# Kernel tuning notes

Measured on AMD Instinct MI355X. Metric: run time of the kernel, lower is better.

## Reference

```python
import jax, jax.numpy as jnp
import numpy as np

N_NODES = 50000
N_GRAPHS = 1024


def _linear_params(key, fan_in, fan_out):
    k1, k2 = jax.random.split(key)
    lim = 1.0 / np.sqrt(fan_in)
    W = jax.random.uniform(k1, (fan_in, fan_out), minval=-lim, maxval=lim, dtype=jnp.float32)
    b = jax.random.uniform(k2, (fan_out,), minval=-lim, maxval=lim, dtype=jnp.float32)
    return W, b


def gcn_conv(x, W, b, src, dst, n):
    # PyG GCNConv: D^{-1/2} (A + I) D^{-1/2} X W + b, deg counted at target after self-loops
    h = x @ W                                   # [N, out]
    deg = jnp.zeros((n,), h.dtype).at[dst].add(1.0) + 1.0
    dinv = jax.lax.rsqrt(deg)
    norm = dinv[src] * dinv[dst]                # [E]
    msg = h[src] * norm[:, None]                # [E, out] (dominant traffic)
    agg = jax.ops.segment_sum(msg, dst, num_segments=n)
    agg = agg + h * (dinv * dinv)[:, None]      # self-loop contribution
    return agg + b


def setup_inputs() -> dict:
    key = jax.random.key(0)
    ks = jax.random.split(key, 16)
    x = jax.random.normal(ks[0], (N_NODES, 64), dtype=jnp.float32)
    edge_index = jax.random.randint(ks[1], (2, 800000), 0, N_NODES, dtype=jnp.int64)
    batch = jnp.sort(jax.random.randint(ks[2], (N_NODES,), 0, N_GRAPHS, dtype=jnp.int64))
    fingerprint_features = jax.random.uniform(ks[3], (N_GRAPHS, 2048), dtype=jnp.float32)
    func_groups = jax.random.uniform(ks[4], (N_GRAPHS, 167), dtype=jnp.float32)
    W1, b1 = _linear_params(ks[5], 64, 128)
    W2, b2 = _linear_params(ks[6], 128, 256)
    W3, b3 = _linear_params(ks[7], 256, 256)
    Wr1, br1 = _linear_params(ks[8], 128, 256)
    Wr2, br2 = _linear_params(ks[9], 256, 256)
    Wfp, bfp = _linear_params(ks[10], 2048, 256)
    Wfg, bfg = _linear_params(ks[11], 167, 256)
    attn_W = jax.random.uniform(ks[12], (256, 256), dtype=jnp.float32)
    Wfc, bfc = _linear_params(ks[13], 256, 1)
    return dict(x=x, edge_index=edge_index, batch=batch,
                fingerprint_features=fingerprint_features, func_groups=func_groups,
                W1=W1, b1=b1, W2=W2, b2=b2, W3=W3, b3=b3,
                Wr1=Wr1, br1=br1, Wr2=Wr2, br2=br2,
                Wfp=Wfp, bfp=bfp, Wfg=Wfg, bfg=bfg,
                attn_W=attn_W, Wfc=Wfc, bfc=bfc)


def reference(x, edge_index, batch, fingerprint_features, func_groups,
              W1, b1, W2, b2, W3, b3, Wr1, br1, Wr2, br2,
              Wfp, bfp, Wfg, bfg, attn_W, Wfc, bfc):
    n = x.shape[0]
    src, dst = edge_index[0], edge_index[1]
    x1 = jax.nn.relu(gcn_conv(x, W1, b1, src, dst, n))            # [N,128]
    # dropout inactive (eval mode)
    x2 = jax.nn.relu(gcn_conv(x1, W2, b2, src, dst, n) + x1 @ Wr1 + br1)  # [N,256]
    x3 = jax.nn.relu(gcn_conv(x2, W3, b3, src, dst, n) + x2 @ Wr2 + br2)  # [N,256]
    fp = jax.nn.relu(fingerprint_features @ Wfp + bfp)            # [B,256]
    fg = jax.nn.relu(func_groups @ Wfg + bfg)                     # [B,256]
    attn = jax.nn.softmax(x3 @ attn_W, axis=1)                    # [N,256]
    xw = attn * x3
    sums = jax.ops.segment_sum(xw, batch, num_segments=N_GRAPHS)  # [B,256]
    cnt = jax.ops.segment_sum(jnp.ones((n,), xw.dtype), batch, num_segments=N_GRAPHS)
    pooled = sums / jnp.maximum(cnt, 1.0)[:, None]                # global_mean_pool
    out = (pooled + fp + fg) @ Wfc + bfc                          # [B,1]
    return out.reshape(-1, 1)
```

## Files before the change

### kernel.cpp

```cpp
#include <hip/hip_runtime.h>
#include <math.h>

#define CDIV(a,b) (((a)+(b)-1)/(b))

typedef __attribute__((ext_vector_type(8))) short bf16x8;
typedef __attribute__((ext_vector_type(4))) float f32x4;

__device__ inline unsigned short f2bf(float f) {
    unsigned int u = __float_as_uint(f);
    u += 0x7fffu + ((u >> 16) & 1u);
    return (unsigned short)(u >> 16);
}
__device__ inline float bf2f(unsigned short h) { return __uint_as_float(((unsigned int)h) << 16); }

__global__ void deg_count_kernel(const int* __restrict__ dst, int* __restrict__ deg, int E) {
    int e = blockIdx.x * blockDim.x + threadIdx.x;
    if (e < E) atomicAdd(&deg[dst[e]], 1);
}

__global__ void dinv_kernel(const int* __restrict__ deg, float* __restrict__ dinv, int N) {
    int i = blockIdx.x * blockDim.x + threadIdx.x;
    if (i < N) dinv[i] = rsqrtf((float)deg[i] + 1.0f);
}

__global__ void scan_kernel(const int* __restrict__ deg, int* __restrict__ off, int N, int E) {
    __shared__ int wsum[16];
    __shared__ int carry_s;
    const int t = threadIdx.x;
    const int lane = t & 63, wid = t >> 6;
    if (t == 0) carry_s = 0;
    __syncthreads();
    for (int base = 0; base < N; base += 1024) {
        int i = base + t;
        int v = (i < N) ? deg[i] : 0;
        int x = v;
        #pragma unroll
        for (int ofs = 1; ofs < 64; ofs <<= 1) {
            int y = __shfl_up(x, ofs, 64);
            if (lane >= ofs) x += y;
        }
        if (lane == 63) wsum[wid] = x;
        __syncthreads();
        if (wid == 0) {
            int wv = (lane < 16) ? wsum[lane] : 0;
            #pragma unroll
            for (int ofs = 1; ofs < 16; ofs <<= 1) {
                int y = __shfl_up(wv, ofs, 64);
                if (lane >= ofs) wv += y;
            }
            if (lane < 16) wsum[lane] = wv;
        }
        __syncthreads();
        int carry = carry_s;
        int wexcl = (wid == 0) ? 0 : wsum[wid - 1];
        int incl = x + wexcl;
        if (i < N) off[i] = carry + incl - v;
        __syncthreads();
        if (t == 1023) carry_s = carry + incl;
        __syncthreads();
    }
    if (t == 0) off[N] = E;
}

__global__ void csr_fill_kernel(const int* __restrict__ src, const int* __restrict__ dst,
                                const int* __restrict__ off, int* __restrict__ pos,
                                int* __restrict__ csr_src, int E) {
    int e = blockIdx.x * blockDim.x + threadIdx.x;
    if (e >= E) return;
    int s = src[e], d = dst[e];
    int p = off[d] + atomicAdd(&pos[d], 1);
    csr_src[p] = s;
}

__global__ void split_kernel(const float* __restrict__ src, unsigned short* __restrict__ hi,
                             unsigned short* __restrict__ lo, long long total) {
    long long idx = (long long)blockIdx.x * blockDim.x + threadIdx.x;
    if (idx >= total) return;
    float v = src[idx];
    unsigned short h = f2bf(v);
    hi[idx] = h;
    lo[idx] = f2bf(v - bf2f(h));
}

__global__ void wsplit_t_kernel(const float* __restrict__ src, int K, int N,
                                unsigned short* __restrict__ dsth, unsigned short* __restrict__ dstl,
                                int ldt, int koff) {
    int idx = blockIdx.x * blockDim.x + threadIdx.x;
    if (idx >= K * N) return;
    int col = idx / K;
    int k = idx - col * K;
    float v = src[(size_t)k * N + col];
    unsigned short h = f2bf(v);
    size_t o = (size_t)col * ldt + koff + k;
    dsth[o] = h;
    dstl[o] = f2bf(v - bf2f(h));
}

__global__ void bsum_kernel(const float* __restrict__ a, const float* __restrict__ b,
                            float* __restrict__ dst, int n) {
    int j = blockIdx.x * blockDim.x + threadIdx.x;
    if (j < n) dst[j] = a[j] + b[j];
}

template<int F, bool PAIRIN>
__global__ __launch_bounds__(F) void gcn_gather_kernel(
        const float* __restrict__ hf, const unsigned short* __restrict__ hih,
        const unsigned short* __restrict__ hil, int ldh, int cofh,
        const float* __restrict__ dinv, const int* __restrict__ off,
        const int* __restrict__ csr_src,
        unsigned short* __restrict__ outh, unsigned short* __restrict__ outl,
        int ldo, int cofo) {
    const int n = blockIdx.x;
    const int j = threadIdx.x;
    float dd = dinv[n];
    auto val = [&](int row) -> float {
        if (PAIRIN) {
            size_t o = (size_t)row * ldh + cofh + j;
            return bf2f(hih[o]) + bf2f(hil[o]);
        } else {
            return hf[(size_t)row * ldh + j];
        }
    };
    float acc = val(n) * dd * dd;
    const int e1 = off[n + 1];
    int e = off[n];
    for (; e + 4 <= e1; e += 4) {
        int s0 = csr_src[e], s1 = csr_src[e + 1], s2 = csr_src[e + 2], s3 = csr_src[e + 3];
        float n0 = dinv[s0] * dd, n1 = dinv[s1] * dd, n2 = dinv[s2] * dd, n3 = dinv[s3] * dd;
        float h0 = val(s0), h1 = val(s1), h2 = val(s2), h3 = val(s3);
        acc += h0 * n0; acc += h1 * n1; acc += h2 * n2; acc += h3 * n3;
    }
    for (; e < e1; ++e) {
        int s0 = csr_src[e];
        acc += val(s0) * (dinv[s0] * dd);
    }
    size_t o = (size_t)n * ldo + cofo + j;
    unsigned short hv = f2bf(acc);
    outh[o] = hv;
    outl[o] = f2bf(acc - bf2f(hv));
}

__global__ __launch_bounds__(256) void mfma_gemm_kernel(
        const unsigned short* __restrict__ Ah, const unsigned short* __restrict__ Al, int lda,
        const unsigned short* __restrict__ Wth, const unsigned short* __restrict__ Wtl, int ldt,
        const float* __restrict__ bias,
        float* __restrict__ Cf32, int ldc,
        unsigned short* __restrict__ outh, unsigned short* __restrict__ outl, int ldo, int coff,
        int M, int K, int NW, int relu, int kchunk) {
    __shared__ unsigned short AsH[128 * 40];
    __shared__ unsigned short AsL[128 * 40];
    __shared__ unsigned short WsH[128 * 40];
    __shared__ unsigned short WsL[128 * 40];
    const int tid = threadIdx.x;
    const int row0 = blockIdx.x * 128;
    const int col0 = blockIdx.y * 128;
    int kbeg = 0, kend = K;
    size_t zoff = 0;
    if (kchunk) {
        kbeg = blockIdx.z * kchunk;
        kend = kbeg + kchunk;
        zoff = (size_t)blockIdx.z * M * NW;
    }
    const int w = tid >> 6, l = tid & 63;
    const int wm = w >> 1, wn = w & 1;
    const int lrow = l & 15, lk = l >> 4;
    f32x4 acc[4][4] = {};
    for (int k0 = kbeg; k0 < kend; k0 += 32) {
        #pragma unroll
        for (int i = 0; i < 2; ++i) {
            int c = tid * 2 + i;
            int r = c >> 2, kq = c & 3;
            int gr = row0 + r;
            uint4 vh = make_uint4(0, 0, 0, 0), vl = make_uint4(0, 0, 0, 0);
            if (gr < M) {
                size_t g = (size_t)gr * lda + k0 + kq * 8;
                vh = *(const uint4*)&Ah[g];
                vl = *(const uint4*)&Al[g];
            }
            *(uint4*)&AsH[r * 40 + kq * 8] = vh;
            *(uint4*)&AsL[r * 40 + kq * 8] = vl;
        }
        #pragma unroll
        for (int i = 0; i < 2; ++i) {
            int c = tid + i * 256;
            int col = c & 127, kq = c >> 7;
            size_t g = (size_t)(col0 + col) * ldt + k0 + kq * 8;
            uint4 vh = *(const uint4*)&Wth[g];
            uint4 vl = *(const uint4*)&Wtl[g];
            *(uint4*)&WsH[col * 40 + kq * 8] = vh;
            *(uint4*)&WsL[col * 40 + kq * 8] = vl;
        }
        __syncthreads();
        bf16x8 aH[4], aL[4], bH[4], bL[4];
        #pragma unroll
        for (int mi = 0; mi < 4; ++mi) {
            int r = wm * 64 + mi * 16 + lrow;
            aH[mi] = *(const bf16x8*)&AsH[r * 40 + lk * 8];
            aL[mi] = *(const bf16x8*)&AsL[r * 40 + lk * 8];
        }
        #pragma unroll
        for (int ni = 0; ni < 4; ++ni) {
            int cc = wn * 64 + ni * 16 + lrow;
            bH[ni] = *(const bf16x8*)&WsH[cc * 40 + lk * 8];
            bL[ni] = *(const bf16x8*)&WsL[cc * 40 + lk * 8];
        }
        #pragma unroll
        for (int mi = 0; mi < 4; ++mi)
            #pragma unroll
            for (int ni = 0; ni < 4; ++ni) {
                acc[mi][ni] = __builtin_amdgcn_mfma_f32_16x16x32_bf16(aH[mi], bH[ni], acc[mi][ni], 0, 0, 0);
                acc[mi][ni] = __builtin_amdgcn_mfma_f32_16x16x32_bf16(aH[mi], bL[ni], acc[mi][ni], 0, 0, 0);
                acc[mi][ni] = __builtin_amdgcn_mfma_f32_16x16x32_bf16(aL[mi], bH[ni], acc[mi][ni], 0, 0, 0);
            }
        __syncthreads();
    }
    #pragma unroll
    for (int mi = 0; mi < 4; ++mi) {
        #pragma unroll
        for (int ni = 0; ni < 4; ++ni) {
            int gc = col0 + wn * 64 + ni * 16 + lrow;
            float bb = bias ? bias[gc] : 0.f;
            #pragma unroll
            for (int q = 0; q < 4; ++q) {
                int gr = row0 + wm * 64 + mi * 16 + lk * 4 + q;
                if (gr >= M) continue;
                float v = acc[mi][ni][q] + bb;
                if (relu) v = fmaxf(v, 0.f);
                if (Cf32) Cf32[zoff + (size_t)gr * ldc + gc] = v;
                if (outh) {
                    size_t o = (size_t)gr * ldo + coff + gc;
                    unsigned short hv = f2bf(v);
                    outh[o] = hv;
                    outl[o] = f2bf(v - bf2f(hv));
                }
            }
        }
    }
}

__global__ void reduce_fp_kernel(const float* __restrict__ part, const float* __restrict__ bias,
                                 float* __restrict__ outp, int total, int stride, int nz) {
    int idx = blockIdx.x * blockDim.x + threadIdx.x;
    if (idx >= total) return;
    float s = 0.f;
    for (int z = 0; z < nz; ++z) s += part[(size_t)z * stride + idx];
    outp[idx] = fmaxf(s + bias[idx & 255], 0.f);
}

__global__ __launch_bounds__(256) void gemm_kernel(
        const float* __restrict__ A, const float* __restrict__ W,
        const float* __restrict__ bias, float* __restrict__ C,
        int M, int K, int N, int do_relu) {
    __shared__ float As[16][128];
    __shared__ float Ws[16][128];
    const int tid = threadIdx.x;
    const int tx = tid & 15;
    const int ty = tid >> 4;
    const int row0 = blockIdx.x * 128;
    const int col0 = blockIdx.y * 128;
    float acc[8][8] = {};
    for (int k0 = 0; k0 < K; k0 += 16) {
        #pragma unroll
        for (int i = 0; i < 2; ++i) {
            int s = tid * 2 + i;
            int r = s >> 2, c = (s & 3) << 2;
            int gr = row0 + r;
            float4 v = make_float4(0.f, 0.f, 0.f, 0.f);
            if (gr < M) {
                if (k0 + c + 3 < K) {
                    v = *(const float4*)(A + (size_t)gr * K + k0 + c);
                } else {
                    float t0 = (k0 + c     < K) ? A[(size_t)gr * K + k0 + c    ] : 0.f;
                    float t1 = (k0 + c + 1 < K) ? A[(size_t)gr * K + k0 + c + 1] : 0.f;
                    float t2 = (k0 + c + 2 < K) ? A[(size_t)gr * K + k0 + c + 2] : 0.f;
                    float t3 = (k0 + c + 3 < K) ? A[(size_t)gr * K + k0 + c + 3] : 0.f;
                    v = make_float4(t0, t1, t2, t3);
                }
            }
            As[c + 0][r] = v.x; As[c + 1][r] = v.y; As[c + 2][r] = v.z; As[c + 3][r] = v.w;
        }
        #pragma unroll
        for (int i = 0; i < 2; ++i) {
            int s = tid * 2 + i;
            int kk = s >> 5, c = (s & 31) << 2;
            int gk = k0 + kk, gc = col0 + c;
            float4 v = make_float4(0.f, 0.f, 0.f, 0.f);
            if (gk < K && gc + 3 < N) v = *(const float4*)(W + (size_t)gk * N + gc);
            *(float4*)&Ws[kk][c] = v;
        }
        __syncthreads();
        #pragma unroll
        for (int kk = 0; kk < 16; ++kk) {
            float a[8], b[8];
            *(float4*)&a[0] = *(const float4*)&As[kk][ty * 4];
            *(float4*)&a[4] = *(const float4*)&As[kk][ty * 4 + 64];
            *(float4*)&b[0] = *(const float4*)&Ws[kk][tx * 4];
            *(float4*)&b[4] = *(const float4*)&Ws[kk][tx * 4 + 64];
            #pragma unroll
            for (int i2 = 0; i2 < 8; ++i2)
                #pragma unroll
                for (int j2 = 0; j2 < 8; ++j2)
                    acc[i2][j2] += a[i2] * b[j2];
        }
        __syncthreads();
    }
    #pragma unroll
    for (int rh = 0; rh < 2; ++rh)
        #pragma unroll
        for (int ii = 0; ii < 4; ++ii) {
            int gr = row0 + ty * 4 + rh * 64 + ii;
            if (gr >= M) continue;
            #pragma unroll
            for (int ch = 0; ch < 2; ++ch) {
                int gc = col0 + tx * 4 + ch * 64;
                float v[4];
                #pragma unroll
                for (int q = 0; q < 4; ++q) {
                    v[q] = acc[rh * 4 + ii][ch * 4 + q] + (bias ? bias[gc + q] : 0.f);
                    if (do_relu) v[q] = fmaxf(v[q], 0.f);
                }
                if (gc + 3 < N)
                    *(float4*)(C + (size_t)gr * N + gc) = make_float4(v[0], v[1], v[2], v[3]);
            }
        }
}

__global__ void softmax256_kernel(float* __restrict__ X, int M) {
    int row = blockIdx.x * 4 + (threadIdx.x >> 6);
    int lane = threadIdx.x & 63;
    if (row >= M) return;
    float* p = X + (size_t)row * 256;
    float v0 = p[lane], v1 = p[lane + 64], v2 = p[lane + 128], v3 = p[lane + 192];
    float m = fmaxf(fmaxf(v0, v1), fmaxf(v2, v3));
    for (int off = 32; off; off >>= 1) m = fmaxf(m, __shfl_xor(m, off));
    v0 = expf(v0 - m); v1 = expf(v1 - m); v2 = expf(v2 - m); v3 = expf(v3 - m);
    float s = v0 + v1 + v2 + v3;
    for (int off = 32; off; off >>= 1) s += __shfl_xor(s, off);
    float inv = 1.0f / s;
    p[lane] = v0 * inv; p[lane + 64] = v1 * inv; p[lane + 128] = v2 * inv; p[lane + 192] = v3 * inv;
}

__global__ __launch_bounds__(256) void pool_kernel(
        const float* __restrict__ attn, const unsigned short* __restrict__ x3h,
        const unsigned short* __restrict__ x3l,
        const int* __restrict__ batch, float* __restrict__ pooled, int N, int B) {
    const int b = blockIdx.x;
    const int j = threadIdx.x;
    int lo = 0, hi = N;
    while (lo < hi) { int m = (lo + hi) >> 1; if (batch[m] < b) lo = m + 1; else hi = m; }
    int s0 = lo;
    hi = N;
    while (lo < hi) { int m = (lo + hi) >> 1; if (batch[m] <= b) lo = m + 1; else hi = m; }
    int s1 = lo;
    float acc = 0.f;
    for (int n = s0; n < s1; ++n) {
        size_t o = (size_t)n * 256 + j;
        acc += attn[o] * (bf2f(x3h[o]) + bf2f(x3l[o]));
    }
    float inv = 1.0f / fmaxf((float)(s1 - s0), 1.0f);
    pooled[(size_t)b * 256 + j] = acc * inv;
}

__global__ void final_kernel(const float* __restrict__ pooled, const float* __restrict__ fp,
                             const float* __restrict__ fg, const float* __restrict__ Wfc,
                             const float* __restrict__ bfc, float* __restrict__ out, int B) {
    int b = blockIdx.x * 4 + (threadIdx.x >> 6);
    int lane = threadIdx.x & 63;
    if (b >= B) return;
    float acc = 0.0f;
    #pragma unroll
    for (int i = 0; i < 4; ++i) {
        int j = lane + i * 64;
        size_t o = (size_t)b * 256 + j;
        acc += (pooled[o] + fp[o] + fg[o]) * Wfc[j];
    }
    for (int off = 32; off; off >>= 1) acc += __shfl_xor(acc, off);
    if (lane == 0) out[b] = acc + bfc[0];
}

extern "C" void kernel_launch(void* const* d_in, const int* in_sizes, int n_in,
                              void* d_out, int out_size, void* d_ws, size_t ws_size,
                              hipStream_t stream) {
    const float* x     = (const float*)d_in[0];
    const int*   ei    = (const int*)d_in[1];
    const int*   batch = (const int*)d_in[2];
    const float* fpin  = (const float*)d_in[3];
    const float* fgin  = (const float*)d_in[4];
    const float* W1  = (const float*)d_in[5];  const float* b1  = (const float*)d_in[6];
    const float* W2  = (const float*)d_in[7];  const float* b2  = (const float*)d_in[8];
    const float* W3  = (const float*)d_in[9];  const float* b3  = (const float*)d_in[10];
    const float* Wr1 = (const float*)d_in[11]; const float* br1 = (const float*)d_in[12];
    const float* Wr2 = (const float*)d_in[13]; const float* br2 = (const float*)d_in[14];
    const float* Wfp = (const float*)d_in[15]; const float* bfp = (const float*)d_in[16];
    const float* Wfg = (const float*)d_in[17]; const float* bfg = (const float*)d_in[18];
    const float* attnW = (const float*)d_in[19];
    const float* Wfc = (const float*)d_in[20]; const float* bfc = (const float*)d_in[21];
    float* out = (float*)d_out;

    const int Nn = in_sizes[0] / 64;
    const int E  = in_sizes[1] / 2;
    const int B  = in_sizes[3] / 2048;
    const int* src = ei;
    const int* dst = ei + E;

    char* wsb = (char*)d_ws;
    size_t woff = 0;
    auto alloc = [&](size_t bytes) -> void* {
        void* p = wsb + woff;
        woff += (bytes + 255) & ~(size_t)255;
        return p;
    };

    int*   deg_i   = (int*)alloc((size_t)Nn * 4);
    int*   pos     = (int*)alloc((size_t)Nn * 4);
    int*   offv    = (int*)alloc(((size_t)Nn + 1) * 4);
    float* dinv    = (float*)alloc((size_t)Nn * 4);
    int*   csr_src = (int*)alloc((size_t)E * 4);
    unsigned short* W1th  = (unsigned short*)alloc(64 * 128 * 2);
    unsigned short* W1tl  = (unsigned short*)alloc(64 * 128 * 2);
    unsigned short* Wc2th = (unsigned short*)alloc(256 * 256 * 2);
    unsigned short* Wc2tl = (unsigned short*)alloc(256 * 256 * 2);
    unsigned short* Wc3th = (unsigned short*)alloc(512 * 256 * 2);
    unsigned short* Wc3tl = (unsigned short*)alloc(512 * 256 * 2);
    unsigned short* aWth  = (unsigned short*)alloc(256 * 256 * 2);
    unsigned short* aWtl  = (unsigned short*)alloc(256 * 256 * 2);
    unsigned short* Wfpth = (unsigned short*)alloc(2048 * 256 * 2);
    unsigned short* Wfptl = (unsigned short*)alloc(2048 * 256 * 2);
    float* bsum2 = (float*)alloc(256 * 4);
    float* bsum3 = (float*)alloc(256 * 4);
    unsigned short* Acat2h = (unsigned short*)alloc((size_t)Nn * 256 * 2);
    unsigned short* Acat2l = (unsigned short*)alloc((size_t)Nn * 256 * 2);
    unsigned short* Acat3h = (unsigned short*)alloc((size_t)Nn * 512 * 2);
    unsigned short* Acat3l = (unsigned short*)alloc((size_t)Nn * 512 * 2);
    unsigned short* x3h    = (unsigned short*)alloc((size_t)Nn * 256 * 2);
    unsigned short* x3l    = (unsigned short*)alloc((size_t)Nn * 256 * 2);
    (void)ws_size; (void)n_in; (void)out_size;

    unsigned short* agg0h = Acat3h;
    unsigned short* agg0l = Acat3l;
    float* logits = (float*)Acat3h;
    char* fpRegion = (char*)Acat3l;
    unsigned short* fpinh = (unsigned short*)(fpRegion);
    unsigned short* fpinl = (unsigned short*)(fpRegion + 4500000 - (4500000 % 256));
    float* part   = (float*)(fpRegion + 9000192);
    float* fpb    = (float*)(fpRegion + 17500160);
    float* fgb    = (float*)(fpRegion + 18600192);
    float* pooled = (float*)(fpRegion + 19700224);

    hipMemsetAsync(deg_i, 0, (size_t)Nn * 4, stream);
    hipMemsetAsync(pos,   0, (size_t)Nn * 4, stream);
    deg_count_kernel<<<CDIV(E, 256), 256, 0, stream>>>(dst, deg_i, E);
    dinv_kernel<<<CDIV(Nn, 256), 256, 0, stream>>>(deg_i, dinv, Nn);
    scan_kernel<<<1, 1024, 0, stream>>>(deg_i, offv, Nn, E);
    csr_fill_kernel<<<CDIV(E, 256), 256, 0, stream>>>(src, dst, offv, pos, csr_src, E);

    wsplit_t_kernel<<<CDIV(64 * 128, 256), 256, 0, stream>>>(W1, 64, 128, W1th, W1tl, 64, 0);
    wsplit_t_kernel<<<CDIV(128 * 256, 256), 256, 0, stream>>>(W2,  128, 256, Wc2th, Wc2tl, 256, 0);
    wsplit_t_kernel<<<CDIV(128 * 256, 256), 256, 0, stream>>>(Wr1, 128, 256, Wc2th, Wc2tl, 256, 128);
    wsplit_t_kernel<<<CDIV(256 * 256, 256), 256, 0, stream>>>(W3,  256, 256, Wc3th, Wc3tl, 512, 0);
    wsplit_t_kernel<<<CDIV(256 * 256, 256), 256, 0, stream>>>(Wr2, 256, 256, Wc3th, Wc3tl, 512, 256);
    wsplit_t_kernel<<<CDIV(256 * 256, 256), 256, 0, stream>>>(attnW, 256, 256, aWth, aWtl, 256, 0);
    wsplit_t_kernel<<<CDIV(2048 * 256, 256), 256, 0, stream>>>(Wfp, 2048, 256, Wfpth, Wfptl, 2048, 0);
    bsum_kernel<<<1, 256, 0, stream>>>(b2, br1, bsum2, 256);
    bsum_kernel<<<1, 256, 0, stream>>>(b3, br2, bsum3, 256);

    const int MB = CDIV(Nn, 128);

    gcn_gather_kernel<64, false><<<Nn, 64, 0, stream>>>(x, nullptr, nullptr, 64, 0,
                                                        dinv, offv, csr_src, agg0h, agg0l, 64, 0);
    mfma_gemm_kernel<<<dim3(MB, 1), 256, 0, stream>>>(agg0h, agg0l, 64, W1th, W1tl, 64,
                                                      b1, nullptr, 0, Acat2h, Acat2l, 256, 128,
                                                      Nn, 64, 128, 1, 0);

    gcn_gather_kernel<128, true><<<Nn, 128, 0, stream>>>(nullptr, Acat2h, Acat2l, 256, 128,
                                                         dinv, offv, csr_src, Acat2h, Acat2l, 256, 0);
    mfma_gemm_kernel<<<dim3(MB, 2), 256, 0, stream>>>(Acat2h, Acat2l, 256, Wc2th, Wc2tl, 256,
                                                      bsum2, nullptr, 0, Acat3h, Acat3l, 512, 256,
                                                      Nn, 256, 256, 1, 0);

    gcn_gather_kernel<256, true><<<Nn, 256, 0, stream>>>(nullptr, Acat3h, Acat3l, 512, 256,
                                                         dinv, offv, csr_src, Acat3h, Acat3l, 512, 0);
    mfma_gemm_kernel<<<dim3(MB, 2), 256, 0, stream>>>(Acat3h, Acat3l, 512, Wc3th, Wc3tl, 512,
                                                      bsum3, nullptr, 0, x3h, x3l, 256, 0,
                                                      Nn, 512, 256, 1, 0);

    mfma_gemm_kernel<<<dim3(MB, 2), 256, 0, stream>>>(x3h, x3l, 256, aWth, aWtl, 256,
                                                      nullptr, logits, 256, nullptr, nullptr, 0, 0,
                                                      Nn, 256, 256, 0, 0);

    long long tfp = (long long)B * 2048;
    split_kernel<<<CDIV(tfp, 256), 256, 0, stream>>>(fpin, fpinh, fpinl, tfp);
    mfma_gemm_kernel<<<dim3(CDIV(B, 128), 2, 8), 256, 0, stream>>>(fpinh, fpinl, 2048, Wfpth, Wfptl, 2048,
                                                                   nullptr, part, 256, nullptr, nullptr, 0, 0,
                                                                   B, 2048, 256, 0, 256);
    reduce_fp_kernel<<<CDIV(B * 256, 256), 256, 0, stream>>>(part, bfp, fpb, B * 256, B * 256, 8);

    gemm_kernel<<<dim3(CDIV(B, 128), 2), 256, 0, stream>>>(fgin, Wfg, bfg, fgb, B, 167, 256, 1);

    softmax256_kernel<<<CDIV(Nn, 4), 256, 0, stream>>>(logits, Nn);
    pool_kernel<<<B, 256, 0, stream>>>(logits, x3h, x3l, batch, pooled, Nn, B);
    final_kernel<<<CDIV(B, 4), 256, 0, stream>>>(pooled, fpb, fgb, Wfc, bfc, out, B);
}
```

Baseline: 838.2 us.

## Gather GCN features in fp16, parallelize CSR scan, fuse softmax into pooling

The GEMM epilogues now also write a compact fp16 copy of each layer's activations, and the edge gather reads that copy instead of the bf16 hi/lo pair or fp32 input. This halves the bytes per gathered row in the dominant random-access traffic. The single-block offset scan is replaced by a three-kernel chunked scan, and softmax is fused into the per-graph pooling kernel, which now also reads x3 in fp16. The cost is fp16 rounding in the aggregation inputs and pooling, extra epilogue stores, and x2/x3 fp16 copies sharing one buffer.

```diff
diff --git a/kernel.cpp b/kernel.cpp
--- a/kernel.cpp
+++ b/kernel.cpp
@@ -12,6 +12,14 @@
     return (unsigned short)(u >> 16);
 }
 __device__ inline float bf2f(unsigned short h) { return __uint_as_float(((unsigned int)h) << 16); }
+__device__ inline unsigned short f2h(float f) {
+    _Float16 h = (_Float16)f;
+    return *(unsigned short*)&h;
+}
+__device__ inline float h2f(unsigned short u) {
+    _Float16 h = *(_Float16*)&u;
+    return (float)h;
+}
 
 __global__ void deg_count_kernel(const int* __restrict__ dst, int* __restrict__ deg, int E) {
     int e = blockIdx.x * blockDim.x + threadIdx.x;
@@ -23,43 +31,50 @@
     if (i < N) dinv[i] = rsqrtf((float)deg[i] + 1.0f);
 }
 
-__global__ void scan_kernel(const int* __restrict__ deg, int* __restrict__ off, int N, int E) {
+__global__ void chunk_sum_kernel(const int* __restrict__ deg, int* __restrict__ csum, int N) {
+    __shared__ int ws[4];
+    int c = blockIdx.x, t = threadIdx.x;
+    int base = c * 1024;
+    int s = 0;
+    for (int i = t; i < 1024; i += 256) { int idx = base + i; s += (idx < N) ? deg[idx] : 0; }
+    for (int o = 32; o; o >>= 1) s += __shfl_xor(s, o);
+    if ((t & 63) == 0) ws[t >> 6] = s;
+    __syncthreads();
+    if (t == 0) csum[c] = ws[0] + ws[1] + ws[2] + ws[3];
+}
+
+__global__ void chunk_scan_kernel(int* __restrict__ csum, int nc) {
+    int t = threadIdx.x;
+    int v = (t < nc) ? csum[t] : 0;
+    int x = v;
+    #pragma unroll
+    for (int o = 1; o < 64; o <<= 1) { int y = __shfl_up(x, o, 64); if (t >= o) x += y; }
+    if (t < nc) csum[t] = x - v;
+}
+
+__global__ void chunk_scan_apply_kernel(const int* __restrict__ deg, const int* __restrict__ cbase,
+                                        int* __restrict__ off, int N, int E) {
     __shared__ int wsum[16];
-    __shared__ int carry_s;
-    const int t = threadIdx.x;
-    const int lane = t & 63, wid = t >> 6;
-    if (t == 0) carry_s = 0;
+    int c = blockIdx.x;
+    int t = threadIdx.x;
+    int lane = t & 63, wid = t >> 6;
+    int i = c * 1024 + t;
+    int v = (i < N) ? deg[i] : 0;
+    int x = v;
+    #pragma unroll
+    for (int o = 1; o < 64; o <<= 1) { int y = __shfl_up(x, o, 64); if (lane >= o) x += y; }
+    if (lane == 63) wsum[wid] = x;
     __syncthreads();
-    for (int base = 0; base < N; base += 1024) {
-        int i = base + t;
-        int v = (i < N) ? deg[i] : 0;
-        int x = v;
-        #pragma unroll
-        for (int ofs = 1; ofs < 64; ofs <<= 1) {
-            int y = __shfl_up(x, ofs, 64);
-            if (lane >= ofs) x += y;
-        }
-        if (lane == 63) wsum[wid] = x;
-        __syncthreads();
-        if (wid == 0) {
-            int wv = (lane < 16) ? wsum[lane] : 0;
-            #pragma unroll
-            for (int ofs = 1; ofs < 16; ofs <<= 1) {
-                int y = __shfl_up(wv, ofs, 64);
-                if (lane >= ofs) wv += y;
-            }
-            if (lane < 16) wsum[lane] = wv;
-        }
-        __syncthreads();
-        int carry = carry_s;
-        int wexcl = (wid == 0) ? 0 : wsum[wid - 1];
-        int incl = x + wexcl;
-        if (i < N) off[i] = carry + incl - v;
-        __syncthreads();
-        if (t == 1023) carry_s = carry + incl;
-        __syncthreads();
-    }
-    if (t == 0) off[N] = E;
+    if (wid == 0) {
+        int wv = (lane < 16) ? wsum[lane] : 0;
+        #pragma unroll
+        for (int o = 1; o < 16; o <<= 1) { int y = __shfl_up(wv, o, 64); if (lane >= o) wv += y; }
+        if (lane < 16) wsum[lane] = wv;
+    }
+    __syncthreads();
+    int wexcl = wid ? wsum[wid - 1] : 0;
+    if (i < N) off[i] = cbase[c] + wexcl + x - v;
+    if (i == N) off[N] = E;
 }
 
 __global__ void csr_fill_kernel(const int* __restrict__ src, const int* __restrict__ dst,
@@ -80,6 +95,13 @@
     unsigned short h = f2bf(v);
     hi[idx] = h;
     lo[idx] = f2bf(v - bf2f(h));
+}
+
+__global__ void f32_to_f16_kernel(const float* __restrict__ src, unsigned short* __restrict__ dst,
+                                  long long total) {
+    long long idx = (long long)blockIdx.x * blockDim.x + threadIdx.x;
+    if (idx >= total) return;
+    dst[idx] = f2h(src[idx]);
 }
 
 __global__ void wsplit_t_kernel(const float* __restrict__ src, int K, int N,
@@ -102,10 +124,9 @@
     if (j < n) dst[j] = a[j] + b[j];
 }
 
-template<int F, bool PAIRIN>
+template<int F>
 __global__ __launch_bounds__(F) void gcn_gather_kernel(
-        const float* __restrict__ hf, const unsigned short* __restrict__ hih,
-        const unsigned short* __restrict__ hil, int ldh, int cofh,
+        const unsigned short* __restrict__ h16, int ldh,
         const float* __restrict__ dinv, const int* __restrict__ off,
         const int* __restrict__ csr_src,
         unsigned short* __restrict__ outh, unsigned short* __restrict__ outl,
@@ -113,26 +134,21 @@
     const int n = blockIdx.x;
     const int j = threadIdx.x;
     float dd = dinv[n];
-    auto val = [&](int row) -> float {
-        if (PAIRIN) {
-            size_t o = (size_t)row * ldh + cofh + j;
-            return bf2f(hih[o]) + bf2f(hil[o]);
-        } else {
-            return hf[(size_t)row * ldh + j];
-        }
-    };
-    float acc = val(n) * dd * dd;
+    float acc = h2f(h16[(size_t)n * ldh + j]) * dd * dd;
     const int e1 = off[n + 1];
     int e = off[n];
     for (; e + 4 <= e1; e += 4) {
         int s0 = csr_src[e], s1 = csr_src[e + 1], s2 = csr_src[e + 2], s3 = csr_src[e + 3];
         float n0 = dinv[s0] * dd, n1 = dinv[s1] * dd, n2 = dinv[s2] * dd, n3 = dinv[s3] * dd;
-        float h0 = val(s0), h1 = val(s1), h2 = val(s2), h3 = val(s3);
+        float h0 = h2f(h16[(size_t)s0 * ldh + j]);
+        float h1 = h2f(h16[(size_t)s1 * ldh + j]);
+        float h2 = h2f(h16[(size_t)s2 * ldh + j]);
+        float h3 = h2f(h16[(size_t)s3 * ldh + j]);
         acc += h0 * n0; acc += h1 * n1; acc += h2 * n2; acc += h3 * n3;
     }
     for (; e < e1; ++e) {
         int s0 = csr_src[e];
-        acc += val(s0) * (dinv[s0] * dd);
+        acc += h2f(h16[(size_t)s0 * ldh + j]) * (dinv[s0] * dd);
     }
     size_t o = (size_t)n * ldo + cofo + j;
     unsigned short hv = f2bf(acc);
@@ -146,6 +162,7 @@
         const float* __restrict__ bias,
         float* __restrict__ Cf32, int ldc,
         unsigned short* __restrict__ outh, unsigned short* __restrict__ outl, int ldo, int coff,
+        unsigned short* __restrict__ outf16, int ldo16,
         int M, int K, int NW, int relu, int kchunk) {
     __shared__ unsigned short AsH[128 * 40];
     __shared__ unsigned short AsL[128 * 40];
@@ -233,6 +250,7 @@
                     outh[o] = hv;
                     outl[o] = f2bf(v - bf2f(hv));
                 }
+                if (outf16) outf16[(size_t)gr * ldo16 + gc] = f2h(v);
             }
         }
     }
@@ -325,40 +343,41 @@
         }
 }
 
-__global__ void softmax256_kernel(float* __restrict__ X, int M) {
-    int row = blockIdx.x * 4 + (threadIdx.x >> 6);
-    int lane = threadIdx.x & 63;
-    if (row >= M) return;
-    float* p = X + (size_t)row * 256;
-    float v0 = p[lane], v1 = p[lane + 64], v2 = p[lane + 128], v3 = p[lane + 192];
-    float m = fmaxf(fmaxf(v0, v1), fmaxf(v2, v3));
-    for (int off = 32; off; off >>= 1) m = fmaxf(m, __shfl_xor(m, off));
-    v0 = expf(v0 - m); v1 = expf(v1 - m); v2 = expf(v2 - m); v3 = expf(v3 - m);
-    float s = v0 + v1 + v2 + v3;
-    for (int off = 32; off; off >>= 1) s += __shfl_xor(s, off);
-    float inv = 1.0f / s;
-    p[lane] = v0 * inv; p[lane + 64] = v1 * inv; p[lane + 128] = v2 * inv; p[lane + 192] = v3 * inv;
-}
-
-__global__ __launch_bounds__(256) void pool_kernel(
-        const float* __restrict__ attn, const unsigned short* __restrict__ x3h,
-        const unsigned short* __restrict__ x3l,
+__global__ __launch_bounds__(256) void softmaxpool_kernel(
+        const float* __restrict__ logits, const unsigned short* __restrict__ x3f16,
         const int* __restrict__ batch, float* __restrict__ pooled, int N, int B) {
+    __shared__ float lacc[4][256];
     const int b = blockIdx.x;
-    const int j = threadIdx.x;
+    const int t = threadIdx.x;
+    const int lane = t & 63, wid = t >> 6;
     int lo = 0, hi = N;
     while (lo < hi) { int m = (lo + hi) >> 1; if (batch[m] < b) lo = m + 1; else hi = m; }
     int s0 = lo;
     hi = N;
     while (lo < hi) { int m = (lo + hi) >> 1; if (batch[m] <= b) lo = m + 1; else hi = m; }
     int s1 = lo;
-    float acc = 0.f;
-    for (int n = s0; n < s1; ++n) {
-        size_t o = (size_t)n * 256 + j;
-        acc += attn[o] * (bf2f(x3h[o]) + bf2f(x3l[o]));
-    }
-    float inv = 1.0f / fmaxf((float)(s1 - s0), 1.0f);
-    pooled[(size_t)b * 256 + j] = acc * inv;
+    float a0 = 0.f, a1 = 0.f, a2 = 0.f, a3 = 0.f;
+    for (int n = s0 + wid; n < s1; n += 4) {
+        const float* p = logits + (size_t)n * 256;
+        float v0 = p[lane], v1 = p[lane + 64], v2 = p[lane + 128], v3 = p[lane + 192];
+        float m = fmaxf(fmaxf(v0, v1), fmaxf(v2, v3));
+        for (int o = 32; o; o >>= 1) m = fmaxf(m, __shfl_xor(m, o));
+        v0 = expf(v0 - m); v1 = expf(v1 - m); v2 = expf(v2 - m); v3 = expf(v3 - m);
+        float s = v0 + v1 + v2 + v3;
+        for (int o = 32; o; o >>= 1) s += __shfl_xor(s, o);
+        float inv = 1.0f / s;
+        const unsigned short* q = x3f16 + (size_t)n * 256;
+        a0 += v0 * inv * h2f(q[lane]);
+        a1 += v1 * inv * h2f(q[lane + 64]);
+        a2 += v2 * inv * h2f(q[lane + 128]);
+        a3 += v3 * inv * h2f(q[lane + 192]);
+    }
+    lacc[wid][lane] = a0; lacc[wid][lane + 64] = a1;
+    lacc[wid][lane + 128] = a2; lacc[wid][lane + 192] = a3;
+    __syncthreads();
+    float tot = lacc[0][t] + lacc[1][t] + lacc[2][t] + lacc[3][t];
+    float invc = 1.0f / fmaxf((float)(s1 - s0), 1.0f);
+    pooled[(size_t)b * 256 + t] = tot * invc;
 }
 
 __global__ void final_kernel(const float* __restrict__ pooled, const float* __restrict__ fp,
@@ -415,6 +434,7 @@
     int*   pos     = (int*)alloc((size_t)Nn * 4);
     int*   offv    = (int*)alloc(((size_t)Nn + 1) * 4);
     float* dinv    = (float*)alloc((size_t)Nn * 4);
+    int*   csum    = (int*)alloc(64 * 4);
     int*   csr_src = (int*)alloc((size_t)E * 4);
     unsigned short* W1th  = (unsigned short*)alloc(64 * 128 * 2);
     unsigned short* W1tl  = (unsigned short*)alloc(64 * 128 * 2);
@@ -434,24 +454,32 @@
     unsigned short* Acat3l = (unsigned short*)alloc((size_t)Nn * 512 * 2);
     unsigned short* x3h    = (unsigned short*)alloc((size_t)Nn * 256 * 2);
     unsigned short* x3l    = (unsigned short*)alloc((size_t)Nn * 256 * 2);
+    unsigned short* x23f16 = (unsigned short*)alloc((size_t)Nn * 256 * 2);
     (void)ws_size; (void)n_in; (void)out_size;
 
     unsigned short* agg0h = Acat3h;
+    unsigned short* xf16  = (unsigned short*)((char*)Acat3h + 8388608);
     unsigned short* agg0l = Acat3l;
+    unsigned short* x1f16 = (unsigned short*)((char*)Acat3l + 8388608);
     float* logits = (float*)Acat3h;
     char* fpRegion = (char*)Acat3l;
     unsigned short* fpinh = (unsigned short*)(fpRegion);
-    unsigned short* fpinl = (unsigned short*)(fpRegion + 4500000 - (4500000 % 256));
+    unsigned short* fpinl = (unsigned short*)(fpRegion + 4499968);
     float* part   = (float*)(fpRegion + 9000192);
     float* fpb    = (float*)(fpRegion + 17500160);
     float* fgb    = (float*)(fpRegion + 18600192);
     float* pooled = (float*)(fpRegion + 19700224);
+    unsigned short* x2f16 = x23f16;
+    unsigned short* x3f16 = x23f16;
 
     hipMemsetAsync(deg_i, 0, (size_t)Nn * 4, stream);
     hipMemsetAsync(pos,   0, (size_t)Nn * 4, stream);
     deg_count_kernel<<<CDIV(E, 256), 256, 0, stream>>>(dst, deg_i, E);
     dinv_kernel<<<CDIV(Nn, 256), 256, 0, stream>>>(deg_i, dinv, Nn);
-    scan_kernel<<<1, 1024, 0, stream>>>(deg_i, offv, Nn, E);
+    const int NC = CDIV(Nn, 1024);
+    chunk_sum_kernel<<<NC, 256, 0, stream>>>(deg_i, csum, Nn);
+    chunk_scan_kernel<<<1, 64, 0, stream>>>(csum, NC);
+    chunk_scan_apply_kernel<<<NC, 1024, 0, stream>>>(deg_i, csum, offv, Nn, E);
     csr_fill_kernel<<<CDIV(E, 256), 256, 0, stream>>>(src, dst, offv, pos, csr_src, E);
 
     wsplit_t_kernel<<<CDIV(64 * 128, 256), 256, 0, stream>>>(W1, 64, 128, W1th, W1tl, 64, 0);
@@ -463,41 +491,41 @@
     wsplit_t_kernel<<<CDIV(2048 * 256, 256), 256, 0, stream>>>(Wfp, 2048, 256, Wfpth, Wfptl, 2048, 0);
     bsum_kernel<<<1, 256, 0, stream>>>(b2, br1, bsum2, 256);
     bsum_kernel<<<1, 256, 0, stream>>>(b3, br2, bsum3, 256);
+    long long txin = (long long)Nn * 64;
+    f32_to_f16_kernel<<<CDIV(txin, 256), 256, 0, stream>>>(x, xf16, txin);
 
     const int MB = CDIV(Nn, 128);
 
-    gcn_gather_kernel<64, false><<<Nn, 64, 0, stream>>>(x, nullptr, nullptr, 64, 0,
-                                                        dinv, offv, csr_src, agg0h, agg0l, 64, 0);
+    gcn_gather_kernel<64><<<Nn, 64, 0, stream>>>(xf16, 64, dinv, offv, csr_src, agg0h, agg0l, 64, 0);
     mfma_gemm_kernel<<<dim3(MB, 1), 256, 0, stream>>>(agg0h, agg0l, 64, W1th, W1tl, 64,
                                                       b1, nullptr, 0, Acat2h, Acat2l, 256, 128,
-                                                      Nn, 64, 128, 1, 0);
-
-    gcn_gather_kernel<128, true><<<Nn, 128, 0, stream>>>(nullptr, Acat2h, Acat2l, 256, 128,
-                                                         dinv, offv, csr_src, Acat2h, Acat2l, 256, 0);
+                                                      x1f16, 128, Nn, 64, 128, 1, 0);
+
+    gcn_gather_kernel<128><<<Nn, 128, 0, stream>>>(x1f16, 128, dinv, offv, csr_src,
+                                                   Acat2h, Acat2l, 256, 0);
     mfma_gemm_kernel<<<dim3(MB, 2), 256, 0, stream>>>(Acat2h, Acat2l, 256, Wc2th, Wc2tl, 256,
                                                       bsum2, nullptr, 0, Acat3h, Acat3l, 512, 256,
-                                                      Nn, 256, 256, 1, 0);
-
-    gcn_gather_kernel<256, true><<<Nn, 256, 0, stream>>>(nullptr, Acat3h, Acat3l, 512, 256,
-                                                         dinv, offv, csr_src, Acat3h, Acat3l, 512, 0);
+                                                      x2f16, 256, Nn, 256, 256, 1, 0);
+
+    gcn_gather_kernel<256><<<Nn, 256, 0, stream>>>(x2f16, 256, dinv, offv, csr_src,
+                                                   Acat3h, Acat3l, 512, 0);
     mfma_gemm_kernel<<<dim3(MB, 2), 256, 0, stream>>>(Acat3h, Acat3l, 512, Wc3th, Wc3tl, 512,
                                                       bsum3, nullptr, 0, x3h, x3l, 256, 0,
-                                                      Nn, 512, 256, 1, 0);
+                                                      x3f16, 256, Nn, 512, 256, 1, 0);
 
     mfma_gemm_kernel<<<dim3(MB, 2), 256, 0, stream>>>(x3h, x3l, 256, aWth, aWtl, 256,
                                                       nullptr, logits, 256, nullptr, nullptr, 0, 0,
-                                                      Nn, 256, 256, 0, 0);
+                                                      nullptr, 0, Nn, 256, 256, 0, 0);
 
     long long tfp = (long long)B * 2048;
     split_kernel<<<CDIV(tfp, 256), 256, 0, stream>>>(fpin, fpinh, fpinl, tfp);
     mfma_gemm_kernel<<<dim3(CDIV(B, 128), 2, 8), 256, 0, stream>>>(fpinh, fpinl, 2048, Wfpth, Wfptl, 2048,
                                                                    nullptr, part, 256, nullptr, nullptr, 0, 0,
-                                                                   B, 2048, 256, 0, 256);
+                                                                   nullptr, 0, B, 2048, 256, 0, 256);
     reduce_fp_kernel<<<CDIV(B * 256, 256), 256, 0, stream>>>(part, bfp, fpb, B * 256, B * 256, 8);
 
     gemm_kernel<<<dim3(CDIV(B, 128), 2), 256, 0, stream>>>(fgin, Wfg, bfg, fgb, B, 167, 256, 1);
 
-    softmax256_kernel<<<CDIV(Nn, 4), 256, 0, stream>>>(logits, Nn);
-    pool_kernel<<<B, 256, 0, stream>>>(logits, x3h, x3l, batch, pooled, Nn, B);
+    softmaxpool_kernel<<<B, 256, 0, stream>>>(logits, x3f16, batch, pooled, Nn, B);
     final_kernel<<<CDIV(B, 4), 256, 0, stream>>>(pooled, fpb, fgb, Wfc, bfc, out, B);
 }
```

After: 759.8 us. 1.1x faster.
